# Kernel optimization log

Measured on AMD Instinct MI355X. Metric: run time of the kernel, lower is better.

## Reference

```python
import jax, jax.numpy as jnp
import numpy as np

N_NODES = 100000   # number of graph nodes
N_EDGES = 1600000  # adjacency nnz (avg degree 16)
FEAT_NNZ = 1600000 # sparse feature nnz (~16 per node)
F_IN = 512
F_OUT = 128


def setup_inputs() -> dict:
    key = jax.random.key(0)
    k1, k2, k3, k4, k5, k6 = jax.random.split(key, 6)
    adj_indices = jax.random.randint(k1, (2, N_EDGES), 0, N_NODES, dtype=jnp.int64 if jax.config.jax_enable_x64 else jnp.int32)
    adj_values = jax.random.uniform(k2, (N_EDGES,), dtype=jnp.float32)
    feat_rows = jax.random.randint(k3, (FEAT_NNZ,), 0, N_NODES)
    feat_cols = jax.random.randint(k4, (FEAT_NNZ,), 0, F_IN)
    feat_values = jax.random.uniform(k5, (FEAT_NNZ,), dtype=jnp.float32)
    # xavier_uniform init of the dense weight, as in the torch module
    bound = float(np.sqrt(6.0 / (F_IN + F_OUT)))
    weight = jax.random.uniform(k6, (F_IN, F_OUT), dtype=jnp.float32, minval=-bound, maxval=bound)
    return {
        "adj_indices": adj_indices,
        "adj_values": adj_values,
        "feat_rows": feat_rows,
        "feat_cols": feat_cols,
        "feat_values": feat_values,
        "weight": weight,
        "num_nodes": N_NODES,
    }


def _spmm(rows, cols, vals, num_rows, dense):
    """COO sparse [num_rows, ?] @ dense [?, K] -> [num_rows, K]."""
    msgs = vals[:, None] * dense[cols]          # [nnz, K] gather + scale
    return jax.ops.segment_sum(msgs, rows, num_segments=num_rows)


def reference(adj_indices, adj_values, feat_rows, feat_cols, feat_values, weight, num_nodes):
    # spmm(features, W): sparse [N, F_in] @ [F_in, F_out]
    base_features = _spmm(feat_rows, feat_cols, feat_values, num_nodes, weight)
    # spmm(A_hat, base): sparse [N, N] @ [N, F_out]  -- neighbor aggregation
    out = _spmm(adj_indices[0], adj_indices[1], adj_values, num_nodes, base_features)
    return out
```

## Files before the change

### kernel.cpp

```cpp
#include <hip/hip_runtime.h>
#include <stdint.h>

#define N_NODES 100000
#define F_IN    512
#define F_OUT   128
#define BROWS   128
#define NBKT    ((N_NODES + BROWS - 1) / BROWS)
#define CAP     2560
#define EPB     4096
#define WPAD    136

typedef unsigned short     u16;
typedef unsigned int       u32;
typedef unsigned long long u64;
typedef long long          i64;

__device__ __forceinline__ float b2f(u16 u) {
    union { u32 i; float f; } x; x.i = ((u32)u) << 16; return x.f;
}
__device__ __forceinline__ u16 f2b(float f) {
    u32 i = __float_as_uint(f);
    return (u16)((i + 0x7fffu + ((i >> 16) & 1u)) >> 16);
}
__device__ __forceinline__ float blo(u32 u) { return __uint_as_float(u << 16); }
__device__ __forceinline__ float bhi(u32 u) { return __uint_as_float(u & 0xFFFF0000u); }
__device__ __forceinline__ int ld_idx(const void* p, int i, int w64) {
    return w64 ? (int)((const i64*)p)[i] : ((const int*)p)[i];
}
__device__ __forceinline__ u16 ld_val_bf(const void* p, int i, int f32) {
    return f32 ? f2b(((const float*)p)[i]) : ((const u16*)p)[i];
}

__device__ __forceinline__ void ld_idx4(int* r, const void* p, int g, int w64) {
    if (w64) {
        const i64* q = (const i64*)p + 4 * (size_t)g;
        longlong2 a = *(const longlong2*)q;
        longlong2 b = *(const longlong2*)(q + 2);
        r[0] = (int)a.x; r[1] = (int)a.y; r[2] = (int)b.x; r[3] = (int)b.y;
    } else {
        int4 a = *(const int4*)((const int*)p + 4 * (size_t)g);
        r[0] = a.x; r[1] = a.y; r[2] = a.z; r[3] = a.w;
    }
}
__device__ __forceinline__ void ld_val4(u32* v, const void* p, int g, int f32) {
    if (f32) {
        float4 a = *(const float4*)((const float*)p + 4 * (size_t)g);
        v[0] = f2b(a.x); v[1] = f2b(a.y); v[2] = f2b(a.z); v[3] = f2b(a.w);
    } else {
        ushort4 a = *(const ushort4*)((const u16*)p + 4 * (size_t)g);
        v[0] = a.x; v[1] = a.y; v[2] = a.z; v[3] = a.w;
    }
}

__device__ __forceinline__ void sniff3(const u16* w, const u32* adj, const u32* frows,
                                       int* sf, int t) {
    if (t < 64) {
        u32 e0 = (w[t]      >> 7) & 0xFF;
        u32 e1 = (w[64 + t] >> 7) & 0xFF;
        u64 bad = __ballot((e0 > 0x7B) || (e1 > 0x7B));
        u64 za = __ballot(adj[2 * t + 1] == 0u);
        u64 zf = __ballot(frows[2 * t + 1] == 0u);
        if (t == 0) {
            sf[0] = (bad != 0);
            sf[1] = (__popcll(za) >= 32);
            sf[2] = (__popcll(zf) >= 32);
        }
    }
}

__global__ __launch_bounds__(512, 4) void binFA2_k(
        const void* __restrict__ frows, const void* __restrict__ fcols,
        const void* __restrict__ fvals, int M, int nFb,
        const void* __restrict__ adjbase, const void* __restrict__ avals, int E,
        const u16* __restrict__ weight,
        int* __restrict__ gcurF, int* __restrict__ gcurA,
        u32* __restrict__ fbkt, u64* __restrict__ abkt) {
    __shared__ int hist[NBKT];
    __shared__ int hbase[NBKT];
    __shared__ int sf[3];
    int t = threadIdx.x;
    sniff3(weight, (const u32*)adjbase, (const u32*)frows, sf, t);
    for (int i = t; i < NBKT; i += 512) hist[i] = 0;
    __syncthreads();
    int f32 = sf[0];
    if ((int)blockIdx.x < nFb) {
        int f64 = sf[2];
        int start = blockIdx.x * EPB;
        int end = min(start + EPB, M);
        int r[8]; int c[8]; u32 v[8];
        #pragma unroll
        for (int h = 0; h < 2; ++h) {
            int g = (start >> 2) + t + h * 512;
            int e0 = 4 * g;
            if (e0 + 3 < end) {
                ld_idx4(r + 4 * h, frows, g, f64);
                ld_idx4(c + 4 * h, fcols, g, f64);
                ld_val4(v + 4 * h, fvals, g, f32);
            } else {
                #pragma unroll
                for (int j = 0; j < 4; ++j) {
                    int jj = 4 * h + j;
                    if (e0 + j < end) {
                        r[jj] = ld_idx(frows, e0 + j, f64);
                        c[jj] = ld_idx(fcols, e0 + j, f64);
                        v[jj] = ld_val_bf(fvals, e0 + j, f32);
                    } else r[jj] = -1;
                }
            }
        }
        #pragma unroll
        for (int j = 0; j < 8; ++j) if (r[j] >= 0) atomicAdd(&hist[r[j] >> 7], 1);
        __syncthreads();
        for (int i = t; i < NBKT; i += 512) {
            int h = hist[i];
            hbase[i] = h ? atomicAdd(&gcurF[i], h) : 0;
            hist[i] = 0;
        }
        __syncthreads();
        #pragma unroll
        for (int j = 0; j < 8; ++j) if (r[j] >= 0) {
            int b = r[j] >> 7;
            int pos = hbase[b] + atomicAdd(&hist[b], 1);
            if (pos < CAP)
                fbkt[(size_t)b * CAP + pos] = (v[j] << 16) | ((u32)(r[j] & 127) << 9) | (u32)c[j];
        }
    } else {
        int a64 = sf[1];
        const void* acols = a64 ? (const void*)((const i64*)adjbase + E)
                                : (const void*)((const int*)adjbase + E);
        int start = ((int)blockIdx.x - nFb) * EPB;
        int end = min(start + EPB, E);
        int r[8]; int c[8]; u32 v[8];
        #pragma unroll
        for (int h = 0; h < 2; ++h) {
            int g = (start >> 2) + t + h * 512;
            int e0 = 4 * g;
            if (e0 + 3 < end) {
                ld_idx4(r + 4 * h, adjbase, g, a64);
                ld_idx4(c + 4 * h, acols, g, a64);
                ld_val4(v + 4 * h, avals, g, f32);
            } else {
                #pragma unroll
                for (int j = 0; j < 4; ++j) {
                    int jj = 4 * h + j;
                    if (e0 + j < end) {
                        r[jj] = ld_idx(adjbase, e0 + j, a64);
                        c[jj] = ld_idx(acols, e0 + j, a64);
                        v[jj] = ld_val_bf(avals, e0 + j, f32);
                    } else r[jj] = -1;
                }
            }
        }
        #pragma unroll
        for (int j = 0; j < 8; ++j) if (r[j] >= 0) atomicAdd(&hist[r[j] >> 7], 1);
        __syncthreads();
        for (int i = t; i < NBKT; i += 512) {
            int h = hist[i];
            hbase[i] = h ? atomicAdd(&gcurA[i], h) : 0;
            hist[i] = 0;
        }
        __syncthreads();
        #pragma unroll
        for (int j = 0; j < 8; ++j) if (r[j] >= 0) {
            int b = r[j] >> 7;
            int pos = hbase[b] + atomicAdd(&hist[b], 1);
            if (pos < CAP)
                abkt[(size_t)b * CAP + pos] =
                    ((u64)v[j] << 24) | ((u64)(r[j] & 127) << 17) | (u64)(u32)c[j];
        }
    }
}

__global__ __launch_bounds__(1024, 1) void stage1_k(const int* __restrict__ cnt,
        const u32* __restrict__ bkts, const void* __restrict__ W,
        const u32* __restrict__ adjsn, const u32* __restrict__ frsn,
        u16* __restrict__ base) {
    __shared__ u16 Wlds[F_IN * WPAD];
    __shared__ u32 csr[CAP];
    __shared__ int hcnt[BROWS];
    __shared__ int roff[BROWS + 1];
    __shared__ int cur[BROWS];
    __shared__ int sf[3];
    int t = threadIdx.x;
    sniff3((const u16*)W, adjsn, frsn, sf, t);
    __syncthreads();
    int f32 = sf[0];
    if (!f32) {
        const u16* Wb = (const u16*)W;
        for (int idx = t; idx < F_IN * 16; idx += 1024) {
            int r = idx >> 4, c = idx & 15;
            uint4 q = *(const uint4*)(Wb + r * F_OUT + c * 8);
            *(uint4*)&Wlds[r * WPAD + c * 8] = q;
        }
    }
    int w = t >> 6, lane = t & 63, g16 = lane >> 4, l16 = lane & 15;
    for (int b = blockIdx.x; b < NBKT; b += gridDim.x) {
        int n = cnt[b]; if (n > CAP) n = CAP;
        const u32* ed = bkts + (size_t)b * CAP;
        if (t < BROWS) hcnt[t] = 0;
        __syncthreads();
        u32 pb[3];
        #pragma unroll
        for (int k = 0; k < 3; ++k) { int i = t + k * 1024; pb[k] = (i < n) ? ed[i] : 0u; }
        #pragma unroll
        for (int k = 0; k < 3; ++k) { int i = t + k * 1024; if (i < n) atomicAdd(&hcnt[(pb[k] >> 9) & 127], 1); }
        __syncthreads();
        if (t < 64) {
            int h0 = hcnt[2 * t], h1 = hcnt[2 * t + 1];
            int s = h0 + h1, v2 = s;
            #pragma unroll
            for (int off = 1; off < 64; off <<= 1) {
                int u = __shfl_up(v2, off);
                if (t >= off) v2 += u;
            }
            int excl = v2 - s;
            roff[2 * t] = excl;     roff[2 * t + 1] = excl + h0;
            cur[2 * t]  = excl;     cur[2 * t + 1]  = excl + h0;
            if (t == 63) roff[128] = v2;
        }
        __syncthreads();
        #pragma unroll
        for (int k = 0; k < 3; ++k) {
            int i = t + k * 1024;
            if (i < n) {
                u32 p = pb[k];
                int pos = atomicAdd(&cur[(p >> 9) & 127], 1);
                csr[pos] = p;
            }
        }
        __syncthreads();
        #pragma unroll
        for (int set = 0; set < 2; ++set) {
            int row = set * 64 + w * 4 + g16;
            int s = roff[row], e = roff[row + 1];
            float a0 = 0.f, a1 = 0.f, a2 = 0.f, a3 = 0.f, a4 = 0.f, a5 = 0.f, a6 = 0.f, a7 = 0.f;
            if (f32) {
                const float* Wf = (const float*)W;
                for (int j0 = s; j0 < e; j0 += 4) {
                    u32 p[4]; float4 qa[4], qb[4];
                    #pragma unroll
                    for (int k = 0; k < 4; ++k) { int jk = j0 + k; p[k] = csr[jk < e ? jk : e - 1]; }
                    #pragma unroll
                    for (int k = 0; k < 4; ++k) {
                        const float* wp = Wf + (size_t)(p[k] & 0x1FF) * F_OUT + l16 * 8;
                        qa[k] = *(const float4*)wp;
                        qb[k] = *(const float4*)(wp + 4);
                    }
                    #pragma unroll
                    for (int k = 0; k < 4; ++k) {
                        float v = (j0 + k < e) ? b2f((u16)(p[k] >> 16)) : 0.f;
                        a0 += v * qa[k].x; a1 += v * qa[k].y;
                        a2 += v * qa[k].z; a3 += v * qa[k].w;
                        a4 += v * qb[k].x; a5 += v * qb[k].y;
                        a6 += v * qb[k].z; a7 += v * qb[k].w;
                    }
                }
            } else {
                for (int j0 = s; j0 < e; j0 += 8) {
                    u32 p[8]; uint4 q[8];
                    #pragma unroll
                    for (int k = 0; k < 8; ++k) { int jk = j0 + k; p[k] = csr[jk < e ? jk : e - 1]; }
                    #pragma unroll
                    for (int k = 0; k < 8; ++k)
                        q[k] = *(const uint4*)&Wlds[(p[k] & 0x1FF) * WPAD + l16 * 8];
                    #pragma unroll
                    for (int k = 0; k < 8; ++k) {
                        float v = (j0 + k < e) ? b2f((u16)(p[k] >> 16)) : 0.f;
                        a0 += v * blo(q[k].x); a1 += v * bhi(q[k].x);
                        a2 += v * blo(q[k].y); a3 += v * bhi(q[k].y);
                        a4 += v * blo(q[k].z); a5 += v * bhi(q[k].z);
                        a6 += v * blo(q[k].w); a7 += v * bhi(q[k].w);
                    }
                }
            }
            int gr = b * BROWS + row;
            if (gr < N_NODES) {
                uint4 o;
                o.x = (u32)f2b(a0) | ((u32)f2b(a1) << 16);
                o.y = (u32)f2b(a2) | ((u32)f2b(a3) << 16);
                o.z = (u32)f2b(a4) | ((u32)f2b(a5) << 16);
                o.w = (u32)f2b(a6) | ((u32)f2b(a7) << 16);
                *(uint4*)(base + (size_t)gr * F_OUT + l16 * 8) = o;
            }
        }
        __syncthreads();
    }
}

__global__ __launch_bounds__(512, 4) void stage2_k(const int* __restrict__ cnt,
        const u64* __restrict__ bkts, const u16* __restrict__ base,
        const void* __restrict__ W, const u32* __restrict__ adjsn,
        const u32* __restrict__ frsn, void* __restrict__ out) {
    __shared__ u64 csr[CAP];
    __shared__ int hcnt[BROWS];
    __shared__ int roff[BROWS + 1];
    __shared__ int cur[BROWS];
    __shared__ int sf[3];
    int t = threadIdx.x;
    sniff3((const u16*)W, adjsn, frsn, sf, t);
    int b = blockIdx.x;
    int n = cnt[b]; if (n > CAP) n = CAP;
    const u64* ed = bkts + (size_t)b * CAP;
    if (t < BROWS) hcnt[t] = 0;
    __syncthreads();
    u64 pb[5];
    #pragma unroll
    for (int k = 0; k < 5; ++k) { int i = t + k * 512; pb[k] = (i < n) ? ed[i] : 0ull; }
    #pragma unroll
    for (int k = 0; k < 5; ++k) { int i = t + k * 512; if (i < n) atomicAdd(&hcnt[(int)((pb[k] >> 17) & 127)], 1); }
    __syncthreads();
    if (t < 64) {
        int h0 = hcnt[2 * t], h1 = hcnt[2 * t + 1];
        int s = h0 + h1, v2 = s;
        #pragma unroll
        for (int off = 1; off < 64; off <<= 1) {
            int u = __shfl_up(v2, off);
            if (t >= off) v2 += u;
        }
        int excl = v2 - s;
        roff[2 * t] = excl;     roff[2 * t + 1] = excl + h0;
        cur[2 * t]  = excl;     cur[2 * t + 1]  = excl + h0;
        if (t == 63) roff[128] = v2;
    }
    __syncthreads();
    #pragma unroll
    for (int k = 0; k < 5; ++k) {
        int i = t + k * 512;
        if (i < n) {
            u64 p = pb[k];
            int pos = atomicAdd(&cur[(int)((p >> 17) & 127)], 1);
            csr[pos] = p;
        }
    }
    __syncthreads();
    int wave = t >> 6, lane = t & 63, g16 = lane >> 4, l16 = lane & 15;
    int f32o = sf[0];
    #pragma unroll
    for (int set = 0; set < 4; ++set) {
        int row = set * 32 + wave * 4 + g16;
        int s = roff[row], e = roff[row + 1];
        float a0 = 0.f, a1 = 0.f, a2 = 0.f, a3 = 0.f, a4 = 0.f, a5 = 0.f, a6 = 0.f, a7 = 0.f;
        for (int j0 = s; j0 < e; j0 += 8) {
            u64 p[8]; uint4 q[8];
            #pragma unroll
            for (int k = 0; k < 8; ++k) { int jk = j0 + k; p[k] = csr[jk < e ? jk : e - 1]; }
            #pragma unroll
            for (int k = 0; k < 8; ++k)
                q[k] = *(const uint4*)(base + (size_t)(u32)(p[k] & 0x1FFFF) * F_OUT + l16 * 8);
            #pragma unroll
            for (int k = 0; k < 8; ++k) {
                float v = (j0 + k < e) ? b2f((u16)(p[k] >> 24)) : 0.f;
                a0 += v * blo(q[k].x); a1 += v * bhi(q[k].x);
                a2 += v * blo(q[k].y); a3 += v * bhi(q[k].y);
                a4 += v * blo(q[k].z); a5 += v * bhi(q[k].z);
                a6 += v * blo(q[k].w); a7 += v * bhi(q[k].w);
            }
        }
        int gr = b * BROWS + row;
        if (gr < N_NODES) {
            if (f32o) {
                float* op = (float*)out + (size_t)gr * F_OUT + l16 * 8;
                float4 o0, o1;
                o0.x = a0; o0.y = a1; o0.z = a2; o0.w = a3;
                o1.x = a4; o1.y = a5; o1.z = a6; o1.w = a7;
                *(float4*)op = o0;
                *(float4*)(op + 4) = o1;
            } else {
                uint4 o;
                o.x = (u32)f2b(a0) | ((u32)f2b(a1) << 16);
                o.y = (u32)f2b(a2) | ((u32)f2b(a3) << 16);
                o.z = (u32)f2b(a4) | ((u32)f2b(a5) << 16);
                o.w = (u32)f2b(a6) | ((u32)f2b(a7) << 16);
                *(uint4*)((u16*)out + (size_t)gr * F_OUT + l16 * 8) = o;
            }
        }
    }
}

extern "C" void kernel_launch(void* const* d_in, const int* in_sizes, int n_in,
                              void* d_out, int out_size, void* d_ws, size_t ws_size,
                              hipStream_t stream) {
    const void* adj_idx   = d_in[0];
    const void* adj_vals  = d_in[1];
    const void* feat_rows = d_in[2];
    const void* feat_cols = d_in[3];
    const void* feat_vals = d_in[4];
    const void* weight    = d_in[5];

    const int E = in_sizes[0] / 2;
    const int M = in_sizes[2];

    char* ws = (char*)d_ws;
    size_t o = 0;
    auto alloc = [&](size_t b) { size_t r = o; o += (b + 255) & ~(size_t)255; return r; };
    int* gcurF = (int*)(ws + alloc((size_t)NBKT * 4));
    int* gcurA = (int*)(ws + alloc((size_t)NBKT * 4));
    size_t cur_end = o;
    u32* fbkt  = (u32*)(ws + alloc((size_t)NBKT * CAP * 4));
    u64* abkt  = (u64*)(ws + alloc((size_t)NBKT * CAP * 8));
    u16* base  = (u16*)(ws + alloc((size_t)N_NODES * F_OUT * 2));
    (void)ws_size;

    const int nFb = (M + EPB - 1) / EPB;
    const int nAb = (E + EPB - 1) / EPB;

    hipMemsetAsync(ws, 0, cur_end, stream);
    binFA2_k<<<nFb + nAb, 512, 0, stream>>>(feat_rows, feat_cols, feat_vals, M, nFb,
                                            adj_idx, adj_vals, E, (const u16*)weight,
                                            gcurF, gcurA, fbkt, abkt);
    stage1_k<<<256, 1024, 0, stream>>>(gcurF, fbkt, weight,
                                       (const u32*)adj_idx, (const u32*)feat_rows, base);
    stage2_k<<<NBKT, 512, 0, stream>>>(gcurA, abkt, base, weight,
                                       (const u32*)adj_idx, (const u32*)feat_rows, d_out);
}
```

Measured before the change: 241.3 us.

## Overlap adjacency binning with stage-1 SpMM and drop LDS weight staging

Splits the combined binning kernel so feature binning runs alone, then fuses adjacency binning with the stage-1 feature SpMM into one launch. Blocks either bin adjacency edges or process one feature bucket, so the two jobs overlap. Stage 1 now uses one 512-thread block per bucket instead of a persistent 1024-thread grid. It reads the bf16 weight from global/L2 instead of a padded 136 KB LDS copy, which cuts shared memory and allows more blocks per CU. The cost is more global weight traffic and an extra launch.

```diff
diff --git a/kernel.cpp b/kernel.cpp
--- a/kernel.cpp
+++ b/kernel.cpp
@@ -8,7 +8,6 @@
 #define NBKT    ((N_NODES + BROWS - 1) / BROWS)
 #define CAP     2560
 #define EPB     4096
-#define WPAD    136
 
 typedef unsigned short     u16;
 typedef unsigned int       u32;
@@ -68,13 +67,11 @@
     }
 }
 
-__global__ __launch_bounds__(512, 4) void binFA2_k(
+__global__ __launch_bounds__(512, 4) void binF_k(
         const void* __restrict__ frows, const void* __restrict__ fcols,
-        const void* __restrict__ fvals, int M, int nFb,
-        const void* __restrict__ adjbase, const void* __restrict__ avals, int E,
-        const u16* __restrict__ weight,
-        int* __restrict__ gcurF, int* __restrict__ gcurA,
-        u32* __restrict__ fbkt, u64* __restrict__ abkt) {
+        const void* __restrict__ fvals, int M,
+        const void* __restrict__ adjbase, const u16* __restrict__ weight,
+        int* __restrict__ gcurF, u32* __restrict__ fbkt) {
     __shared__ int hist[NBKT];
     __shared__ int hbase[NBKT];
     __shared__ int sf[3];
@@ -82,53 +79,70 @@
     sniff3(weight, (const u32*)adjbase, (const u32*)frows, sf, t);
     for (int i = t; i < NBKT; i += 512) hist[i] = 0;
     __syncthreads();
-    int f32 = sf[0];
-    if ((int)blockIdx.x < nFb) {
-        int f64 = sf[2];
-        int start = blockIdx.x * EPB;
-        int end = min(start + EPB, M);
-        int r[8]; int c[8]; u32 v[8];
-        #pragma unroll
-        for (int h = 0; h < 2; ++h) {
-            int g = (start >> 2) + t + h * 512;
-            int e0 = 4 * g;
-            if (e0 + 3 < end) {
-                ld_idx4(r + 4 * h, frows, g, f64);
-                ld_idx4(c + 4 * h, fcols, g, f64);
-                ld_val4(v + 4 * h, fvals, g, f32);
-            } else {
-                #pragma unroll
-                for (int j = 0; j < 4; ++j) {
-                    int jj = 4 * h + j;
-                    if (e0 + j < end) {
-                        r[jj] = ld_idx(frows, e0 + j, f64);
-                        c[jj] = ld_idx(fcols, e0 + j, f64);
-                        v[jj] = ld_val_bf(fvals, e0 + j, f32);
-                    } else r[jj] = -1;
-                }
-            }
-        }
-        #pragma unroll
-        for (int j = 0; j < 8; ++j) if (r[j] >= 0) atomicAdd(&hist[r[j] >> 7], 1);
+    int f32 = sf[0], f64 = sf[2];
+    int start = blockIdx.x * EPB;
+    int end = min(start + EPB, M);
+    int r[8]; int c[8]; u32 v[8];
+    #pragma unroll
+    for (int h = 0; h < 2; ++h) {
+        int g = (start >> 2) + t + h * 512;
+        int e0 = 4 * g;
+        if (e0 + 3 < end) {
+            ld_idx4(r + 4 * h, frows, g, f64);
+            ld_idx4(c + 4 * h, fcols, g, f64);
+            ld_val4(v + 4 * h, fvals, g, f32);
+        } else {
+            #pragma unroll
+            for (int j = 0; j < 4; ++j) {
+                int jj = 4 * h + j;
+                if (e0 + j < end) {
+                    r[jj] = ld_idx(frows, e0 + j, f64);
+                    c[jj] = ld_idx(fcols, e0 + j, f64);
+                    v[jj] = ld_val_bf(fvals, e0 + j, f32);
+                } else r[jj] = -1;
+            }
+        }
+    }
+    #pragma unroll
+    for (int j = 0; j < 8; ++j) if (r[j] >= 0) atomicAdd(&hist[r[j] >> 7], 1);
+    __syncthreads();
+    for (int i = t; i < NBKT; i += 512) {
+        int h = hist[i];
+        hbase[i] = h ? atomicAdd(&gcurF[i], h) : 0;
+        hist[i] = 0;
+    }
+    __syncthreads();
+    #pragma unroll
+    for (int j = 0; j < 8; ++j) if (r[j] >= 0) {
+        int b = r[j] >> 7;
+        int pos = hbase[b] + atomicAdd(&hist[b], 1);
+        if (pos < CAP)
+            fbkt[(size_t)b * CAP + pos] = (v[j] << 16) | ((u32)(r[j] & 127) << 9) | (u32)c[j];
+    }
+}
+
+union S1Mem {
+    struct { int hist[NBKT]; int hbase[NBKT]; } bin;
+    struct { u32 csr[CAP]; int hcnt[BROWS]; int roff[BROWS + 1]; int cur[BROWS]; } s1;
+};
+
+__global__ __launch_bounds__(512, 4) void binAs1_k(
+        const void* __restrict__ adjbase, const void* __restrict__ avals, int E, int nAb,
+        const u32* __restrict__ frsn, const u16* __restrict__ weight,
+        int* __restrict__ gcurA, u64* __restrict__ abkt,
+        const int* __restrict__ cntF, const u32* __restrict__ fbkt,
+        const void* __restrict__ W, u16* __restrict__ base) {
+    __shared__ S1Mem sm;
+    __shared__ int sf[3];
+    int t = threadIdx.x;
+    sniff3(weight, (const u32*)adjbase, frsn, sf, t);
+    if ((int)blockIdx.x < nAb) {
+        for (int i = t; i < NBKT; i += 512) sm.bin.hist[i] = 0;
         __syncthreads();
-        for (int i = t; i < NBKT; i += 512) {
-            int h = hist[i];
-            hbase[i] = h ? atomicAdd(&gcurF[i], h) : 0;
-            hist[i] = 0;
-        }
-        __syncthreads();
-        #pragma unroll
-        for (int j = 0; j < 8; ++j) if (r[j] >= 0) {
-            int b = r[j] >> 7;
-            int pos = hbase[b] + atomicAdd(&hist[b], 1);
-            if (pos < CAP)
-                fbkt[(size_t)b * CAP + pos] = (v[j] << 16) | ((u32)(r[j] & 127) << 9) | (u32)c[j];
-        }
-    } else {
-        int a64 = sf[1];
+        int f32 = sf[0], a64 = sf[1];
         const void* acols = a64 ? (const void*)((const i64*)adjbase + E)
                                 : (const void*)((const int*)adjbase + E);
-        int start = ((int)blockIdx.x - nFb) * EPB;
+        int start = blockIdx.x * EPB;
         int end = min(start + EPB, E);
         int r[8]; int c[8]; u32 v[8];
         #pragma unroll
@@ -152,138 +166,115 @@
             }
         }
         #pragma unroll
-        for (int j = 0; j < 8; ++j) if (r[j] >= 0) atomicAdd(&hist[r[j] >> 7], 1);
+        for (int j = 0; j < 8; ++j) if (r[j] >= 0) atomicAdd(&sm.bin.hist[r[j] >> 7], 1);
         __syncthreads();
         for (int i = t; i < NBKT; i += 512) {
-            int h = hist[i];
-            hbase[i] = h ? atomicAdd(&gcurA[i], h) : 0;
-            hist[i] = 0;
+            int h = sm.bin.hist[i];
+            sm.bin.hbase[i] = h ? atomicAdd(&gcurA[i], h) : 0;
+            sm.bin.hist[i] = 0;
         }
         __syncthreads();
         #pragma unroll
         for (int j = 0; j < 8; ++j) if (r[j] >= 0) {
             int b = r[j] >> 7;
-            int pos = hbase[b] + atomicAdd(&hist[b], 1);
+            int pos = sm.bin.hbase[b] + atomicAdd(&sm.bin.hist[b], 1);
             if (pos < CAP)
                 abkt[(size_t)b * CAP + pos] =
                     ((u64)v[j] << 24) | ((u64)(r[j] & 127) << 17) | (u64)(u32)c[j];
         }
-    }
-}
-
-__global__ __launch_bounds__(1024, 1) void stage1_k(const int* __restrict__ cnt,
-        const u32* __restrict__ bkts, const void* __restrict__ W,
-        const u32* __restrict__ adjsn, const u32* __restrict__ frsn,
-        u16* __restrict__ base) {
-    __shared__ u16 Wlds[F_IN * WPAD];
-    __shared__ u32 csr[CAP];
-    __shared__ int hcnt[BROWS];
-    __shared__ int roff[BROWS + 1];
-    __shared__ int cur[BROWS];
-    __shared__ int sf[3];
-    int t = threadIdx.x;
-    sniff3((const u16*)W, adjsn, frsn, sf, t);
+        return;
+    }
+    int b = blockIdx.x - nAb;
+    int n = cntF[b]; if (n > CAP) n = CAP;
+    const u32* ed = fbkt + (size_t)b * CAP;
+    if (t < BROWS) sm.s1.hcnt[t] = 0;
     __syncthreads();
     int f32 = sf[0];
-    if (!f32) {
-        const u16* Wb = (const u16*)W;
-        for (int idx = t; idx < F_IN * 16; idx += 1024) {
-            int r = idx >> 4, c = idx & 15;
-            uint4 q = *(const uint4*)(Wb + r * F_OUT + c * 8);
-            *(uint4*)&Wlds[r * WPAD + c * 8] = q;
-        }
-    }
-    int w = t >> 6, lane = t & 63, g16 = lane >> 4, l16 = lane & 15;
-    for (int b = blockIdx.x; b < NBKT; b += gridDim.x) {
-        int n = cnt[b]; if (n > CAP) n = CAP;
-        const u32* ed = bkts + (size_t)b * CAP;
-        if (t < BROWS) hcnt[t] = 0;
-        __syncthreads();
-        u32 pb[3];
+    u32 pb[5];
+    #pragma unroll
+    for (int k = 0; k < 5; ++k) { int i = t + k * 512; pb[k] = (i < n) ? ed[i] : 0u; }
+    #pragma unroll
+    for (int k = 0; k < 5; ++k) { int i = t + k * 512; if (i < n) atomicAdd(&sm.s1.hcnt[(pb[k] >> 9) & 127], 1); }
+    __syncthreads();
+    if (t < 64) {
+        int h0 = sm.s1.hcnt[2 * t], h1 = sm.s1.hcnt[2 * t + 1];
+        int s = h0 + h1, v2 = s;
         #pragma unroll
-        for (int k = 0; k < 3; ++k) { int i = t + k * 1024; pb[k] = (i < n) ? ed[i] : 0u; }
-        #pragma unroll
-        for (int k = 0; k < 3; ++k) { int i = t + k * 1024; if (i < n) atomicAdd(&hcnt[(pb[k] >> 9) & 127], 1); }
-        __syncthreads();
-        if (t < 64) {
-            int h0 = hcnt[2 * t], h1 = hcnt[2 * t + 1];
-            int s = h0 + h1, v2 = s;
-            #pragma unroll
-            for (int off = 1; off < 64; off <<= 1) {
-                int u = __shfl_up(v2, off);
-                if (t >= off) v2 += u;
-            }
-            int excl = v2 - s;
-            roff[2 * t] = excl;     roff[2 * t + 1] = excl + h0;
-            cur[2 * t]  = excl;     cur[2 * t + 1]  = excl + h0;
-            if (t == 63) roff[128] = v2;
-        }
-        __syncthreads();
-        #pragma unroll
-        for (int k = 0; k < 3; ++k) {
-            int i = t + k * 1024;
-            if (i < n) {
-                u32 p = pb[k];
-                int pos = atomicAdd(&cur[(p >> 9) & 127], 1);
-                csr[pos] = p;
-            }
-        }
-        __syncthreads();
-        #pragma unroll
-        for (int set = 0; set < 2; ++set) {
-            int row = set * 64 + w * 4 + g16;
-            int s = roff[row], e = roff[row + 1];
-            float a0 = 0.f, a1 = 0.f, a2 = 0.f, a3 = 0.f, a4 = 0.f, a5 = 0.f, a6 = 0.f, a7 = 0.f;
-            if (f32) {
-                const float* Wf = (const float*)W;
-                for (int j0 = s; j0 < e; j0 += 4) {
-                    u32 p[4]; float4 qa[4], qb[4];
-                    #pragma unroll
-                    for (int k = 0; k < 4; ++k) { int jk = j0 + k; p[k] = csr[jk < e ? jk : e - 1]; }
-                    #pragma unroll
-                    for (int k = 0; k < 4; ++k) {
-                        const float* wp = Wf + (size_t)(p[k] & 0x1FF) * F_OUT + l16 * 8;
-                        qa[k] = *(const float4*)wp;
-                        qb[k] = *(const float4*)(wp + 4);
-                    }
-                    #pragma unroll
-                    for (int k = 0; k < 4; ++k) {
-                        float v = (j0 + k < e) ? b2f((u16)(p[k] >> 16)) : 0.f;
-                        a0 += v * qa[k].x; a1 += v * qa[k].y;
-                        a2 += v * qa[k].z; a3 += v * qa[k].w;
-                        a4 += v * qb[k].x; a5 += v * qb[k].y;
-                        a6 += v * qb[k].z; a7 += v * qb[k].w;
-                    }
+        for (int off = 1; off < 64; off <<= 1) {
+            int u = __shfl_up(v2, off);
+            if (t >= off) v2 += u;
+        }
+        int excl = v2 - s;
+        sm.s1.roff[2 * t] = excl;     sm.s1.roff[2 * t + 1] = excl + h0;
+        sm.s1.cur[2 * t]  = excl;     sm.s1.cur[2 * t + 1]  = excl + h0;
+        if (t == 63) sm.s1.roff[128] = v2;
+    }
+    __syncthreads();
+    #pragma unroll
+    for (int k = 0; k < 5; ++k) {
+        int i = t + k * 512;
+        if (i < n) {
+            u32 p = pb[k];
+            int pos = atomicAdd(&sm.s1.cur[(p >> 9) & 127], 1);
+            sm.s1.csr[pos] = p;
+        }
+    }
+    __syncthreads();
+    int wave = t >> 6, lane = t & 63, g16 = lane >> 4, l16 = lane & 15;
+    #pragma unroll
+    for (int set = 0; set < 4; ++set) {
+        int row = set * 32 + wave * 4 + g16;
+        int s = sm.s1.roff[row], e = sm.s1.roff[row + 1];
+        float a0 = 0.f, a1 = 0.f, a2 = 0.f, a3 = 0.f, a4 = 0.f, a5 = 0.f, a6 = 0.f, a7 = 0.f;
+        if (f32) {
+            const float* Wf = (const float*)W;
+            for (int j0 = s; j0 < e; j0 += 4) {
+                u32 p[4]; float4 qa[4], qb[4];
+                #pragma unroll
+                for (int k = 0; k < 4; ++k) { int jk = j0 + k; p[k] = sm.s1.csr[jk < e ? jk : e - 1]; }
+                #pragma unroll
+                for (int k = 0; k < 4; ++k) {
+                    const float* wp = Wf + (size_t)(p[k] & 0x1FF) * F_OUT + l16 * 8;
+                    qa[k] = *(const float4*)wp;
+                    qb[k] = *(const float4*)(wp + 4);
                 }
-            } else {
-                for (int j0 = s; j0 < e; j0 += 8) {
-                    u32 p[8]; uint4 q[8];
-                    #pragma unroll
-                    for (int k = 0; k < 8; ++k) { int jk = j0 + k; p[k] = csr[jk < e ? jk : e - 1]; }
-                    #pragma unroll
-                    for (int k = 0; k < 8; ++k)
-                        q[k] = *(const uint4*)&Wlds[(p[k] & 0x1FF) * WPAD + l16 * 8];
-                    #pragma unroll
-                    for (int k = 0; k < 8; ++k) {
-                        float v = (j0 + k < e) ? b2f((u16)(p[k] >> 16)) : 0.f;
-                        a0 += v * blo(q[k].x); a1 += v * bhi(q[k].x);
-                        a2 += v * blo(q[k].y); a3 += v * bhi(q[k].y);
-                        a4 += v * blo(q[k].z); a5 += v * bhi(q[k].z);
-                        a6 += v * blo(q[k].w); a7 += v * bhi(q[k].w);
-                    }
+                #pragma unroll
+                for (int k = 0; k < 4; ++k) {
+                    float v = (j0 + k < e) ? b2f((u16)(p[k] >> 16)) : 0.f;
+                    a0 += v * qa[k].x; a1 += v * qa[k].y;
+                    a2 += v * qa[k].z; a3 += v * qa[k].w;
+                    a4 += v * qb[k].x; a5 += v * qb[k].y;
+                    a6 += v * qb[k].z; a7 += v * qb[k].w;
                 }
             }
-            int gr = b * BROWS + row;
-            if (gr < N_NODES) {
-                uint4 o;
-                o.x = (u32)f2b(a0) | ((u32)f2b(a1) << 16);
-                o.y = (u32)f2b(a2) | ((u32)f2b(a3) << 16);
-                o.z = (u32)f2b(a4) | ((u32)f2b(a5) << 16);
-                o.w = (u32)f2b(a6) | ((u32)f2b(a7) << 16);
-                *(uint4*)(base + (size_t)gr * F_OUT + l16 * 8) = o;
-            }
-        }
-        __syncthreads();
+        } else {
+            const u16* Wb = (const u16*)W;
+            for (int j0 = s; j0 < e; j0 += 8) {
+                u32 p[8]; uint4 q[8];
+                #pragma unroll
+                for (int k = 0; k < 8; ++k) { int jk = j0 + k; p[k] = sm.s1.csr[jk < e ? jk : e - 1]; }
+                #pragma unroll
+                for (int k = 0; k < 8; ++k)
+                    q[k] = *(const uint4*)(Wb + (size_t)(p[k] & 0x1FF) * F_OUT + l16 * 8);
+                #pragma unroll
+                for (int k = 0; k < 8; ++k) {
+                    float v = (j0 + k < e) ? b2f((u16)(p[k] >> 16)) : 0.f;
+                    a0 += v * blo(q[k].x); a1 += v * bhi(q[k].x);
+                    a2 += v * blo(q[k].y); a3 += v * bhi(q[k].y);
+                    a4 += v * blo(q[k].z); a5 += v * bhi(q[k].z);
+                    a6 += v * blo(q[k].w); a7 += v * bhi(q[k].w);
+                }
+            }
+        }
+        int gr = b * BROWS + row;
+        if (gr < N_NODES) {
+            uint4 o;
+            o.x = (u32)f2b(a0) | ((u32)f2b(a1) << 16);
+            o.y = (u32)f2b(a2) | ((u32)f2b(a3) << 16);
+            o.z = (u32)f2b(a4) | ((u32)f2b(a5) << 16);
+            o.w = (u32)f2b(a6) | ((u32)f2b(a7) << 16);
+            *(uint4*)(base + (size_t)gr * F_OUT + l16 * 8) = o;
+        }
     }
 }
 
@@ -405,11 +396,11 @@
     const int nAb = (E + EPB - 1) / EPB;
 
     hipMemsetAsync(ws, 0, cur_end, stream);
-    binFA2_k<<<nFb + nAb, 512, 0, stream>>>(feat_rows, feat_cols, feat_vals, M, nFb,
-                                            adj_idx, adj_vals, E, (const u16*)weight,
-                                            gcurF, gcurA, fbkt, abkt);
-    stage1_k<<<256, 1024, 0, stream>>>(gcurF, fbkt, weight,
-                                       (const u32*)adj_idx, (const u32*)feat_rows, base);
+    binF_k<<<nFb, 512, 0, stream>>>(feat_rows, feat_cols, feat_vals, M,
+                                    adj_idx, (const u16*)weight, gcurF, fbkt);
+    binAs1_k<<<nAb + NBKT, 512, 0, stream>>>(adj_idx, adj_vals, E, nAb,
+                                             (const u32*)feat_rows, (const u16*)weight,
+                                             gcurA, abkt, gcurF, fbkt, weight, base);
     stage2_k<<<NBKT, 512, 0, stream>>>(gcurA, abkt, base, weight,
                                        (const u32*)adj_idx, (const u32*)feat_rows, d_out);
 }
```

Result: no change. 237.1 us (-1.7%).
